# Kernel optimization log

Measured on AMD Instinct MI355X. Metric: run time of the kernel, lower is better.

## Reference

```python
import jax, jax.numpy as jnp
import numpy as np

EPS_OT = 0.05   # sinkhorn epsilon
ITERS = 3       # sinkhorn iterations
NH = 8          # attention heads


def _l2norm(x, axis):
    return x / jnp.maximum(jnp.linalg.norm(x, axis=axis, keepdims=True), 1e-12)


def _conv(x, w, pad):
    return jax.lax.conv_general_dilated(
        x, w, (1, 1), ((pad, pad), (pad, pad)),
        dimension_numbers=("NCHW", "OIHW", "NCHW"))


def _head(x, w1, b1, g, beta, w2, b2):
    # Conv3x3 -> BatchNorm (train-mode batch stats) -> ReLU -> Conv1x1
    h = _conv(x, w1, 1) + b1[None, :, None, None]
    mu = jnp.mean(h, (0, 2, 3), keepdims=True)
    var = jnp.var(h, (0, 2, 3), keepdims=True)
    h = jax.nn.relu((h - mu) / jnp.sqrt(var + 1e-5) * g[None, :, None, None]
                    + beta[None, :, None, None])
    return jnp.einsum("oc,bchw->bohw", w2, h) + b2[None, :, None, None]


def setup_inputs() -> dict:
    key = jax.random.key(0)
    ks = jax.random.split(key, 20)
    B, C, H, W, TD = 8, 256, 48, 48, 512
    s = 0.02
    f32 = jnp.float32
    d = {
        "img_feat": jax.random.normal(ks[0], (B, C, H, W), f32),
        "txt_feat": jax.random.normal(ks[1], (B, TD), f32),
        "density_map": jax.random.uniform(ks[2], (B, 1, H, W), f32),
        "tp_w": s * jax.random.normal(ks[3], (C, TD), f32), "tp_b": jnp.zeros((C,), f32),
        "wq": s * jax.random.normal(ks[4], (C, C), f32), "bq": jnp.zeros((C,), f32),
        "wk": s * jax.random.normal(ks[5], (C, C), f32), "bk": jnp.zeros((C,), f32),
        "wv": s * jax.random.normal(ks[6], (C, C), f32), "bv": jnp.zeros((C,), f32),
        "wo": s * jax.random.normal(ks[7], (C, C), f32), "bo": jnp.zeros((C,), f32),
        "ln_g": jnp.ones((C,), f32), "ln_b": jnp.zeros((C,), f32),
        "op_w": s * jax.random.normal(ks[8], (C, C), f32), "op_b": jnp.zeros((C,), f32),
        "h1_w": s * jax.random.normal(ks[9], (C // 2, C, 3, 3), f32), "h1_b": jnp.zeros((C // 2,), f32),
        "h_bn_g": jnp.ones((C // 2,), f32), "h_bn_b": jnp.zeros((C // 2,), f32),
        "h2_w": s * jax.random.normal(ks[10], (2, C // 2), f32), "h2_b": jnp.zeros((2,), f32),
        "v1_w": s * jax.random.normal(ks[11], (C // 2, C, 3, 3), f32), "v1_b": jnp.zeros((C // 2,), f32),
        "v_bn_g": jnp.ones((C // 2,), f32), "v_bn_b": jnp.zeros((C // 2,), f32),
        "v2_w": s * jax.random.normal(ks[12], (2, C // 2), f32), "v2_b": jnp.zeros((2,), f32),
        "temperature": 0.07 * jnp.ones((1,), f32),
        "spatial_weight": 0.1 * jnp.ones((1,), f32),
    }
    return d


def reference(img_feat, txt_feat, density_map, tp_w, tp_b, wq, bq, wk, bk,
              wv, bv, wo, bo, ln_g, ln_b, op_w, op_b, h1_w, h1_b, h_bn_g,
              h_bn_b, h2_w, h2_b, v1_w, v1_b, v_bn_g, v_bn_b, v2_w, v2_b,
              temperature, spatial_weight):
    B, C, H, W = img_feat.shape
    N = H * W
    hd = C // NH

    # ---- text projection (single text token) ----
    txt_emb = txt_feat @ tp_w.T + tp_b                      # [B,C]

    # ---- cross attention: query = pixels, key/value = 1 text token ----
    img_flat = img_feat.reshape(B, C, N).transpose(0, 2, 1)  # [B,N,C]
    q = (img_flat @ wq.T + bq).reshape(B, N, NH, hd)
    k = (txt_emb @ wk.T + bk).reshape(B, 1, NH, hd)
    v = (txt_emb @ wv.T + bv).reshape(B, 1, NH, hd)
    scores = jnp.einsum("bnhd,bkhd->bhnk", q, k) / jnp.sqrt(jnp.float32(hd))
    attn = jax.nn.softmax(scores, axis=-1)                  # ones (k len = 1)
    ctx = jnp.einsum("bhnk,bkhd->bnhd", attn, v).reshape(B, N, C)
    attn_out = ctx @ wo.T + bo

    # ---- residual + layernorm ----
    x = img_flat + attn_out
    mu = jnp.mean(x, -1, keepdims=True)
    var = jnp.var(x, -1, keepdims=True)
    source_feat = (x - mu) / jnp.sqrt(var + 1e-5) * ln_g + ln_b   # [B,N,C]
    mod_img_feat = source_feat.transpose(0, 2, 1).reshape(B, C, H, W)

    # ---- target distribution q from density map ----
    target = jax.nn.relu(density_map.reshape(B, N)) + 1e-6
    q_dist = target / jnp.sum(target, axis=1, keepdims=True)

    # ---- source distribution p from cosine similarity ----
    img_n = _l2norm(mod_img_feat, 1)                        # [B,C,H,W]
    txt_n = _l2norm(txt_emb, 1)                             # [B,C]
    cos = jnp.sum(img_n * txt_n[:, :, None, None], axis=1).reshape(B, N)
    temp = jnp.clip(temperature, 0.01, None)                # [1]
    logits = cos / temp
    mask = (cos > 0.0).astype(jnp.float32)
    shifted = logits - jnp.max(logits, axis=1, keepdims=True)
    p_un = jnp.exp(shifted) * mask + 1e-8
    p = p_un / jnp.sum(p_un, axis=1, keepdims=True)

    # ---- cost matrix: feature + spatial ----
    src_n = _l2norm(source_feat, 2)                         # [B,N,C]
    feature_cost = 1.0 - jnp.einsum("bnc,bmc->bnm", src_n, src_n)
    gy, gx = jnp.meshgrid(jnp.linspace(0.0, 1.0, H), jnp.linspace(0.0, 1.0, W),
                          indexing="ij")
    coords = jnp.stack([gy, gx], -1).reshape(N, 2)
    d2 = jnp.sum((coords[:, None, :] - coords[None, :, :]) ** 2, -1)
    spatial_cost = jnp.sqrt(jnp.maximum(d2, 0.0)) / 1.41421356  # [N,N]
    cost = feature_cost + spatial_weight * spatial_cost[None]   # [B,N,N]

    # ---- log-domain Sinkhorn ----
    log_p = jnp.log(p + 1e-12)
    log_q = jnp.log(q_dist + 1e-12)
    f = jnp.zeros_like(p)
    g = jnp.zeros_like(q_dist)
    for _ in range(ITERS):
        f = EPS_OT * (log_p - jax.scipy.special.logsumexp(
            (g[:, None, :] - cost) / EPS_OT, axis=2))
        g = EPS_OT * (log_q - jax.scipy.special.logsumexp(
            (f[:, :, None] - cost) / EPS_OT, axis=1))
    T = jnp.exp((f[:, :, None] + g[:, None, :] - cost) / EPS_OT)

    # ---- transport features: T^T @ source ----
    fused = jnp.einsum("bnm,bnc->bmc", T, source_feat)      # [B,N,C]
    fused_feat = fused.transpose(0, 2, 1).reshape(B, C, H, W)

    out_feat = img_feat + (jnp.einsum("oc,bchw->bohw", op_w, fused_feat)
                           + op_b[None, :, None, None])
    heatmap_logits = _head(out_feat, h1_w, h1_b, h_bn_g, h_bn_b, h2_w, h2_b)
    hv_logits = _head(out_feat, v1_w, v1_b, v_bn_g, v_bn_b, v2_w, v2_b)
    return out_feat, heatmap_logits, hv_logits
```

## Files before the change

kernel.cpp:

```cpp
#include <hip/hip_runtime.h>
#include <hip/hip_bf16.h>

#define NTOK 2304
#define CCH  256
#define BB   8
#define NSPL 2

typedef __attribute__((ext_vector_type(4))) float f32x4;
typedef __attribute__((ext_vector_type(8))) short s16x8;
typedef __attribute__((ext_vector_type(8))) _Float16 h16x8;
typedef unsigned short u16;
typedef unsigned char u8;

__device__ __forceinline__ u16 f2bf(float x){
  union{float f; unsigned u;} v; v.f = x;
  unsigned r = v.u + 0x7fffu + ((v.u>>16)&1u);
  return (u16)(r>>16);
}
__device__ __forceinline__ float bf2f(u16 h){
  union{float f; unsigned u;} v; v.u = ((unsigned)h)<<16; return v.f;
}

#if __has_builtin(__builtin_amdgcn_cvt_f32_fp8) && __has_builtin(__builtin_amdgcn_cvt_pk_fp8_f32)
#define HWFP8 1
#else
#define HWFP8 0
#endif

__device__ __forceinline__ u8 enc8(float z){
  union{float f; unsigned u;} a; a.f = fabsf(z) * 0x1p-120f;
  unsigned u = a.u + 0x7FFFFu + ((a.u>>20)&1u);
  unsigned b = (u>>20)&0x7Fu;
  if (b > 0x7Eu) b = 0x7Eu;
  return (u8)(b | (z<0.f ? 0x80u : 0u));
}
__device__ __forceinline__ float dec8(unsigned b){
  union{unsigned u; float f;} w;
  w.u = ((b&0x80u)<<24) | ((b&0x7Fu)<<20);
  return w.f * 0x1p120f;
}

#if HWFP8
__device__ __forceinline__ float DEC8(unsigned w, int e){
  switch(e & 3){
    case 0:  return __builtin_amdgcn_cvt_f32_fp8((int)w, 0);
    case 1:  return __builtin_amdgcn_cvt_f32_fp8((int)w, 1);
    case 2:  return __builtin_amdgcn_cvt_f32_fp8((int)w, 2);
    default: return __builtin_amdgcn_cvt_f32_fp8((int)w, 3);
  }
}
__device__ __forceinline__ unsigned pack4(float z0,float z1,float z2,float z3){
  int v = __builtin_amdgcn_cvt_pk_fp8_f32(z0, z1, 0, false);
  v = __builtin_amdgcn_cvt_pk_fp8_f32(z2, z3, v, true);
  return (unsigned)v;
}
#else
__device__ __forceinline__ float DEC8(unsigned w, int e){
  return dec8((w>>(8*(e&3)))&0xFFu);
}
__device__ __forceinline__ unsigned pack4(float z0,float z1,float z2,float z3){
  return (unsigned)enc8(z0) | ((unsigned)enc8(z1)<<8) |
         ((unsigned)enc8(z2)<<16) | ((unsigned)enc8(z3)<<24);
}
#endif

__device__ __forceinline__ int swz512(int row, int b){ return row*512 + (b ^ ((row&7)<<4)); }
__device__ __forceinline__ int swz128(int row, int b){ return row*128 + (b ^ ((row&7)<<4)); }
__device__ __forceinline__ int swz64 (int row, int b){ return row*64  + (b ^ ((row&3)<<4)); }

__device__ __forceinline__ void gl_lds16(const void* g, void* l){
  __builtin_amdgcn_global_load_lds(
      (const __attribute__((address_space(1))) unsigned int*)g,
      (__attribute__((address_space(3))) unsigned int*)l, 16, 0, 0);
}

struct CanonArgs {
  const void* src[31];
  int n[31];
  int off[31];
};

__global__ void k_detect(const u16* probe, int* flag){
  if (threadIdx.x==0){
    int cnt=0;
    for (int i=0;i<16;++i){
      unsigned e = (probe[2*i]>>7)&0xFFu;
      if (e>=100u && e<=140u) ++cnt;
    }
    *flag = (cnt>=14)?1:0;
  }
}

__global__ __launch_bounds__(256) void k_canon(CanonArgs a, float* dst, const int* flag, int nt){
  int t = blockIdx.y;
  if (t>=nt) return;
  int n = a.n[t];
  const void* s = a.src[t];
  float* d = dst + a.off[t];
  bool isbf = (*flag)!=0;
  int n4 = n >> 2;
  for (int i = blockIdx.x*256+threadIdx.x; i < n4; i += gridDim.x*256){
    if (isbf){
      ushort4 v = ((const ushort4*)s)[i];
      float4 o; o.x=bf2f(v.x); o.y=bf2f(v.y); o.z=bf2f(v.z); o.w=bf2f(v.w);
      ((float4*)d)[i] = o;
    } else {
      ((float4*)d)[i] = ((const float4*)s)[i];
    }
  }
  int base = n4<<2;
  int rem = n - base;
  int i = blockIdx.x*256+threadIdx.x;
  if (i < rem)
    d[base+i] = isbf ? bf2f(((const u16*)s)[base+i]) : ((const float*)s)[base+i];
}

__global__ __launch_bounds__(256) void k_zero(float* p, int n4){
  int i = blockIdx.x*256+threadIdx.x;
  if (i < n4) ((float4*)p)[i] = (float4){0.f,0.f,0.f,0.f};
}

__global__ __launch_bounds__(256) void k_txt(const float* txt, const float* tpw, const float* tpb,
    const float* wv, const float* bv, const float* wo, const float* bo, float* TXTN, float* AVEC){
  int b=blockIdx.x, t=threadIdx.x;
  __shared__ float sT[512];
  __shared__ float sE[256];
  __shared__ float sV[256];
  __shared__ float red[4];
  sT[t]      = txt[b*512+t];
  sT[t+256]  = txt[b*512+256+t];
  __syncthreads();
  float acc = tpb[t];
  const float* wr = tpw + (size_t)t*512;
  for (int k=0;k<512;++k) acc = fmaf(sT[k], wr[k], acc);
  sE[t] = acc;
  float ss = acc*acc;
  for (int d=1; d<64; d<<=1) ss += __shfl_xor(ss, d);
  if ((t&63)==0) red[t>>6] = ss;
  __syncthreads();
  float nrm = sqrtf(red[0]+red[1]+red[2]+red[3]);
  TXTN[b*256+t] = acc / fmaxf(nrm, 1e-12f);
  float av = bv[t];
  const float* wvr = wv + (size_t)t*256;
  for (int k=0;k<256;++k) av = fmaf(sE[k], wvr[k], av);
  sV[t] = av;
  __syncthreads();
  float ao = bo[t];
  const float* wor = wo + (size_t)t*256;
  for (int k=0;k<256;++k) ao = fmaf(sV[k], wor[k], ao);
  AVEC[b*256+t] = ao;
}

__global__ __launch_bounds__(256) void k_lnfuse(const float* img, const float* AVEC, const float* lng,
    const float* lnb, const float* TXTN, u16* SF, u16* SN, float* COS){
  int b=blockIdx.y, n0=blockIdx.x*32, t=threadIdx.x;
  __shared__ float xt[32][256];
  float av = AVEC[b*256+t];
  const float* ip = img + ((size_t)b*256 + t)*NTOK + n0;
  #pragma unroll
  for (int j4=0;j4<8;++j4){
    float4 v = *(const float4*)(ip + j4*4);
    xt[j4*4+0][t]=v.x+av; xt[j4*4+1][t]=v.y+av; xt[j4*4+2][t]=v.z+av; xt[j4*4+3][t]=v.w+av;
  }
  int wv_=t>>6, l=t&63;
  float lg[4], lb[4], tn[4];
  #pragma unroll
  for (int k=0;k<4;++k){ lg[k]=lng[l+64*k]; lb[k]=lnb[l+64*k]; tn[k]=TXTN[b*256+l+64*k]; }
  __syncthreads();
  for (int rr=0; rr<8; ++rr){
    int j = wv_*8+rr; int n = n0+j;
    float x[4]; float s=0.f, ss=0.f;
    #pragma unroll
    for (int k=0;k<4;++k){ float v=xt[j][l+64*k]; x[k]=v; s+=v; ss=fmaf(v,v,ss); }
    for (int d=1; d<64; d<<=1){ s += __shfl_xor(s,d); ss += __shfl_xor(ss,d); }
    float mu = s*(1.f/256.f);
    float var = ss*(1.f/256.f) - mu*mu;
    float rstd = rsqrtf(fmaxf(var,0.f)+1e-5f);
    float y[4]; float sy=0.f;
    #pragma unroll
    for (int k=0;k<4;++k){ y[k] = fmaf((x[k]-mu)*rstd, lg[k], lb[k]); sy = fmaf(y[k],y[k],sy); }
    for (int d=1; d<64; d<<=1) sy += __shfl_xor(sy,d);
    float rn = 1.f/fmaxf(sqrtf(sy),1e-12f);
    float cp = 0.f;
    size_t base = ((size_t)b*NTOK + n)*CCH;
    #pragma unroll
    for (int k=0;k<4;++k){
      float sv = y[k]*rn;
      SF[base + l+64*k] = f2bf(y[k]);
      SN[base + l+64*k] = f2bf(sv);
      cp = fmaf(sv, tn[k], cp);
    }
    for (int d=1; d<64; d<<=1) cp += __shfl_xor(cp,d);
    if (l==0) COS[b*NTOK+n] = cp;
  }
}

__global__ __launch_bounds__(256) void k_pqred(const float* COS, const float* den, const float* tmpp, float* PQS){
  int b=blockIdx.x, t=threadIdx.x;
  __shared__ float red[256];
  float temp = fmaxf(tmpp[0], 0.01f);
  float mx = -1e30f;
  for (int n=t; n<NTOK; n+=256) mx = fmaxf(mx, COS[b*NTOK+n]);
  red[t]=mx; __syncthreads();
  for (int o=128;o>0;o>>=1){ if (t<o) red[t]=fmaxf(red[t],red[t+o]); __syncthreads(); }
  float maxc = red[0]; __syncthreads();
  float sp=0.f, st=0.f;
  for (int n=t; n<NTOK; n+=256){
    float cv = COS[b*NTOK+n];
    sp += __expf((cv-maxc)/temp)*((cv>0.f)?1.f:0.f)+1e-8f;
    float dv = den[b*NTOK+n];
    st += fmaxf(dv,0.f)+1e-6f;
  }
  red[t]=sp; __syncthreads();
  for (int o=128;o>0;o>>=1){ if (t<o) red[t]+=red[t+o]; __syncthreads(); }
  sp = red[0]; __syncthreads();
  red[t]=st; __syncthreads();
  for (int o=128;o>0;o>>=1){ if (t<o) red[t]+=red[t+o]; __syncthreads(); }
  if (t==0){ PQS[b*4]=maxc; PQS[b*4+1]=sp; PQS[b*4+2]=red[0]; }
}

__global__ __launch_bounds__(256) void k_pqelem(const float* COS, const float* den, const float* tmpp,
    const float* PQS, float* LOGP, float* LOGQ, float* GV, float* CY, float* CX){
  int idx = blockIdx.x*256+threadIdx.x;
  float temp = fmaxf(tmpp[0], 0.01f);
  if (idx < BB*NTOK){
    int b = idx / NTOK;
    float maxc = PQS[b*4], sp = PQS[b*4+1], st = PQS[b*4+2];
    float cv = COS[idx];
    float pu = __expf((cv-maxc)/temp)*((cv>0.f)?1.f:0.f)+1e-8f;
    LOGP[idx] = logf(pu/sp + 1e-12f);
    float dv = den[idx];
    LOGQ[idx] = logf((fmaxf(dv,0.f)+1e-6f)/st + 1e-12f);
    GV[idx] = 0.f;
  }
  if (idx < NTOK){
    int h = idx/48, w = idx - h*48;
    CY[idx] = (float)h*(1.f/47.f);
    CX[idx] = (float)w*(1.f/47.f);
  }
}

__global__ __launch_bounds__(256) void k_packw(const float* h1w, const float* v1w, u16* W1P){
  int idx = blockIdx.x*256+threadIdx.x;
  int head = idx / 294912;
  int rem = idx - head*294912;
  int oc = rem / 2304;
  int k = rem - oc*2304;
  int tap = k >> 8;
  int c = k & 255;
  const float* src = head ? v1w : h1w;
  W1P[idx] = f2bf(src[(oc*256 + c)*9 + tap]);
}

__global__ __launch_bounds__(256) void k_trans(const u16* SF, u16* SFT){
  int n0 = blockIdx.x*64, c0 = blockIdx.y*64, b = blockIdx.z;
  __shared__ u16 tl[64][68];
  int t = threadIdx.x;
  int nl = t>>3, c8 = (t&7)*8;
  #pragma unroll
  for (int p=0;p<2;++p){
    int n = nl + p*32;
    s16x8 v = *(const s16x8*)(SF + ((size_t)(b*NTOK + n0+n)*CCH + c0 + c8));
    #pragma unroll
    for (int e=0;e<8;++e) tl[c8+e][n] = (u16)v[e];
  }
  __syncthreads();
  int cl = t>>3, n8 = (t&7)*8;
  #pragma unroll
  for (int p=0;p<2;++p){
    int c = cl + p*32;
    union{ s16x8 v; u16 us[8]; } pk;
    #pragma unroll
    for (int e=0;e<8;++e){ int s = n8+e; pk.us[e] = tl[c][((s&3)<<4) | (s>>2)]; }
    *(s16x8*)(SFT + ((size_t)(b*CCH + c0+c)*NTOK + n0 + n8)) = pk.v;
  }
}

__global__ __launch_bounds__(256, 4) void k_cost(const u16* SN, const float* CY, const float* CX,
    const float* swp, u8* Z, float* PZ, int b_base){
  int zb = blockIdx.z, b = b_base + zb;
  int i0 = blockIdx.x*64, by = blockIdx.y, j0b = by*256;
  const u16* SNb = SN + (size_t)b*NTOK*CCH;
  u8* Zb = Z + (size_t)zb*NTOK*NTOK;
  __shared__ __align__(16) char Bs[64*512];
  int tid=threadIdx.x, w=tid>>6, l=tid&63, g4=l>>4, lc=l&15;
  float spw = swp[0]*(20.0f/1.41421356f);
  const u16* Arow = SNb + (size_t)(i0 + w*16 + lc)*CCH + g4*8;
  s16x8 af[8];
  #pragma unroll
  for (int ks=0; ks<8; ++ks) af[ks] = *(const s16x8*)(Arow + ks*32);
  int mrow = w*16 + g4*4;
  float cyi[4], cxi[4];
  #pragma unroll
  for (int r=0;r<4;++r){ int i = i0+mrow+r; cyi[r]=CY[i]; cxi[r]=CX[i]; }
  float Srow[4] = {0.f,0.f,0.f,0.f};
  for (int js=0; js<4; ++js){
    int j0 = j0b + js*64;
    __syncthreads();
    #pragma unroll
    for (int u=0; u<8; ++u){
      int row = u*8 + w*2 + (l>>5);
      int src = ((l&31)*16) ^ ((row&7)<<4);
      gl_lds16((const char*)(SNb + (size_t)(j0+row)*CCH) + src, Bs + u*4096 + w*1024);
    }
    __syncthreads();
    f32x4 acc[4];
    #pragma unroll
    for (int cf=0;cf<4;++cf) acc[cf] = (f32x4){0.f,0.f,0.f,0.f};
    #pragma unroll
    for (int ks=0; ks<8; ++ks){
      int kb = ks*64 + g4*16;
      #pragma unroll
      for (int cf=0; cf<4; ++cf){
        s16x8 bb = *(const s16x8*)(Bs + swz512(cf*16+lc, kb));
        acc[cf] = __builtin_amdgcn_mfma_f32_16x16x32_bf16(af[ks], bb, acc[cf], 0,0,0);
      }
    }
    float zf[4][4];
    #pragma unroll
    for (int cf=0; cf<4; ++cf){
      int j = j0 + cf*16 + lc;
      float cyj = CY[j], cxj = CX[j];
      #pragma unroll
      for (int r=0;r<4;++r){
        float dy = cyi[r]-cyj, dx = cxi[r]-cxj;
        zf[cf][r] = (acc[cf][r]-1.0f)*20.0f - spw*sqrtf(fmaf(dy,dy,dx*dx));
      }
    }
    size_t zrow = (size_t)(i0+mrow)*NTOK + j0 + lc*4;
    #pragma unroll
    for (int r=0;r<4;++r){
      unsigned pw = pack4(zf[0][r], zf[1][r], zf[2][r], zf[3][r]);
      Srow[r] += __expf(DEC8(pw,0)) + __expf(DEC8(pw,1))
               + __expf(DEC8(pw,2)) + __expf(DEC8(pw,3));
      *(unsigned*)(Zb + zrow + (size_t)r*NTOK) = pw;
    }
  }
  #pragma unroll
  for (int r=0;r<4;++r){
    float s = Srow[r];
    s += __shfl_xor(s,1); s += __shfl_xor(s,2); s += __shfl_xor(s,4); s += __shfl_xor(s,8);
    if (lc==0) PZ[(size_t)(zb*NTOK + i0 + mrow + r)*9 + by] = s;
  }
}

__global__ __launch_bounds__(256) void k_sinkred(const float* PZ, const float* LOGP, float* FV,
    int b_base, int zcnt){
  int idx = blockIdx.x*256 + threadIdx.x;
  if (idx >= zcnt*NTOK) return;
  int zb = idx / NTOK, row = idx - zb*NTOK, b = b_base + zb;
  const float* p = PZ + (size_t)idx*9;
  float s = 0.f;
  #pragma unroll
  for (int k=0;k<9;++k) s += p[k];
  FV[b*NTOK+row] = 0.05f*(LOGP[b*NTOK+row] - logf(s));
}

__global__ __launch_bounds__(256) void k_sinkZ(const u8* Z, const float* addv,
    const float* basev, float* outv, int b_base){
  int zb = blockIdx.y, b = b_base + zb, i0 = blockIdx.x*32;
  __shared__ float fs[NTOK];
  __shared__ float wm[4];
  int t = threadIdx.x;
  for (int j=t; j<NTOK; j+=256){
    int p = j & 63, tt = ((p&3)<<4) | (p>>2);
    fs[j] = addv[b*NTOK + (j & ~63) + tt]*20.f;
  }
  __syncthreads();
  float m = -1e30f;
  for (int j=t; j<NTOK; j+=256) m = fmaxf(m, fs[j]);
  #pragma unroll
  for (int d=1; d<64; d<<=1) m = fmaxf(m, __shfl_xor(m, d));
  if ((t&63)==0) wm[t>>6] = m;
  __syncthreads();
  float C = fmaxf(fmaxf(wm[0],wm[1]), fmaxf(wm[2],wm[3]));
  int rl = t>>3, q = t&7;
  int row = i0 + rl;
  const u8* zr = Z + ((size_t)zb*NTOK + row)*NTOK;
  float S = 0.f;
  for (int c0 = q*32; c0 < NTOK; c0 += 256){
    uint4 zA = *(const uint4*)(zr + c0);
    uint4 zB = *(const uint4*)(zr + c0 + 16);
    unsigned wd[8] = {zA.x,zA.y,zA.z,zA.w, zB.x,zB.y,zB.z,zB.w};
    float s32 = 0.f;
    #pragma unroll
    for (int k=0;k<8;++k)
      #pragma unroll
      for (int e=0;e<4;++e)
        s32 += __expf(fs[c0 + k*4 + e] + DEC8(wd[k], e) - C);
    S += s32;
  }
  #pragma unroll
  for (int d=1; d<8; d<<=1) S += __shfl_xor(S, d);
  if (q==0)
    outv[b*NTOK+row] = 0.05f*(basev[b*NTOK+row] - (C + logf(S)));
}

__global__ __launch_bounds__(256, 3) void k_applyT(const u8* Z, const u16* SFT, const float* FVv,
    const float* GVv, float* FUF, int b_base){
  int zb = blockIdx.z, b = b_base + zb, m0 = blockIdx.x*64;
  int sp = blockIdx.y;
  int nbeg = sp*(NTOK/NSPL), nend = nbeg + (NTOK/NSPL);
  __shared__ __align__(16) char WtL[64*128];
  __shared__ __align__(16) char BL[256*128];
  __shared__ float gs[64];
  __shared__ float sfv[NTOK/NSPL];
  int tid=threadIdx.x, w=tid>>6, l=tid&63, g4=l>>4, lc=l&15;
  if (tid<64) gs[tid] = GVv[b*NTOK+m0+tid]*20.f;
  const float* Fv = FVv + b*NTOK;
  for (int j=tid; j<NTOK/NSPL; j+=256){
    int jj = nbeg + j;
    int p = jj & 63, tt = ((p&3)<<4) | (p>>2);
    sfv[j] = Fv[(jj & ~63) + tt]*20.f;
  }
  const u8* Zb = Z + ((size_t)zb*NTOK + m0)*NTOK;
  const u16* SFTb = SFT + (size_t)b*CCH*NTOK;
  f32x4 acc[4][4];
  #pragma unroll
  for (int mf=0;mf<4;++mf)
    #pragma unroll
    for (int cf=0;cf<4;++cf) acc[mf][cf] = (f32x4){0.f,0.f,0.f,0.f};
  int zm = tid>>2, zq = (tid&3)*16;
  int lrow = l>>3;
  int lsrc = ((l&7)*16) ^ (lrow<<4);
  uint4 zwc = *(const uint4*)(Zb + (size_t)zm*NTOK + nbeg + zq);
  for (int n0=nbeg; n0<nend; n0+=64){
    __syncthreads();
    int nn = (n0+64 < nend) ? n0+64 : nbeg;
    uint4 zwn = *(const uint4*)(Zb + (size_t)zm*NTOK + nn + zq);
    #pragma unroll
    for (int u=0; u<8; ++u){
      int row = w*64 + u*8 + lrow;
      gl_lds16((const char*)(SFTb + (size_t)row*NTOK) + n0*2 + lsrc,
               BL + (w*64 + u*8)*128);
    }
    {
      float g20 = gs[zm];
      unsigned wd[4] = {zwc.x, zwc.y, zwc.z, zwc.w};
      union{ s16x8 v; u16 us[8]; } w0, w1;
      int sbase = n0 - nbeg + zq;
      #pragma unroll
      for (int col=0; col<16; ++col){
        float val = __expf(sfv[sbase+col] + g20 + DEC8(wd[col>>2], col&3));
        if (col < 8) w0.us[col] = f2bf(val); else w1.us[col-8] = f2bf(val);
      }
      *(s16x8*)(WtL + swz128(zm, zq*2)) = w0.v;
      *(s16x8*)(WtL + swz128(zm, zq*2+16)) = w1.v;
    }
    __syncthreads();
    #pragma unroll
    for (int kk=0; kk<2; ++kk){
      s16x8 a[4];
      #pragma unroll
      for (int mf=0;mf<4;++mf) a[mf] = *(const s16x8*)(WtL + swz128(mf*16+lc, kk*64 + g4*16));
      #pragma unroll
      for (int cf=0; cf<4; ++cf){
        s16x8 bb = *(const s16x8*)(BL + swz128(w*64+cf*16+lc, kk*64 + g4*16));
        #pragma unroll
        for (int mf=0; mf<4; ++mf)
          acc[mf][cf] = __builtin_amdgcn_mfma_f32_16x16x32_bf16(a[mf], bb, acc[mf][cf], 0,0,0);
      }
    }
    zwc = zwn;
  }
  float* FUb = FUF + (size_t)b*NTOK*CCH;
  #pragma unroll
  for (int mf=0; mf<4; ++mf)
    #pragma unroll
    for (int cf=0; cf<4; ++cf)
      #pragma unroll
      for (int r=0;r<4;++r){
        int m = m0 + mf*16 + g4*4 + r;
        int c = w*64 + cf*16 + lc;
        atomicAdd(&FUb[(size_t)m*CCH + c], acc[mf][cf][r]);
      }
}

__global__ __launch_bounds__(256) void k_opgemm(const float* FUF, const float* opw, const float* opb,
    const float* img, float* dout, u16* OFN){
  int b=blockIdx.y, n0=blockIdx.x*64;
  __shared__ __align__(16) char Am[64*512];
  __shared__ __align__(16) char Bw[256*64];
  int tid=threadIdx.x, w=tid>>6, l=tid&63, g4=l>>4, lc=l&15;
  const float* FUb = FUF + (size_t)b*NTOK*CCH;
  for (int ch=tid; ch<64*32; ch+=256){
    int r=ch>>5, c8=(ch&31)*8;
    const float* fp = FUb + (size_t)(n0+r)*CCH + c8;
    float4 v0 = *(const float4*)fp;
    float4 v1 = *(const float4*)(fp+4);
    union { s16x8 v; u16 us[8]; } pk;
    pk.us[0]=f2bf(v0.x); pk.us[1]=f2bf(v0.y); pk.us[2]=f2bf(v0.z); pk.us[3]=f2bf(v0.w);
    pk.us[4]=f2bf(v1.x); pk.us[5]=f2bf(v1.y); pk.us[6]=f2bf(v1.z); pk.us[7]=f2bf(v1.w);
    *(s16x8*)(Am + swz512(r, c8*2)) = pk.v;
  }
  f32x4 acc[4][4];
  #pragma unroll
  for (int mf=0;mf<4;++mf)
    #pragma unroll
    for (int cf=0;cf<4;++cf) acc[mf][cf] = (f32x4){0.f,0.f,0.f,0.f};
  for (int ks=0; ks<8; ++ks){
    __syncthreads();
    {
      int o = tid;
      const float* wr = opw + (size_t)o*CCH + ks*32;
      #pragma unroll
      for (int u=0; u<4; ++u){
        float4 v0 = *(const float4*)(wr + u*8);
        float4 v1 = *(const float4*)(wr + u*8 + 4);
        union { s16x8 v; u16 us[8]; } pk;
        pk.us[0]=f2bf(v0.x); pk.us[1]=f2bf(v0.y); pk.us[2]=f2bf(v0.z); pk.us[3]=f2bf(v0.w);
        pk.us[4]=f2bf(v1.x); pk.us[5]=f2bf(v1.y); pk.us[6]=f2bf(v1.z); pk.us[7]=f2bf(v1.w);
        *(s16x8*)(Bw + swz64(o, u*16)) = pk.v;
      }
    }
    __syncthreads();
    #pragma unroll
    for (int mf=0; mf<4; ++mf){
      s16x8 a = *(const s16x8*)(Am + swz512(mf*16+lc, (ks*32+g4*8)*2));
      #pragma unroll
      for (int cf=0; cf<4; ++cf){
        int o = w*64+cf*16+lc;
        s16x8 bb = *(const s16x8*)(Bw + swz64(o, g4*16));
        acc[mf][cf] = __builtin_amdgcn_mfma_f32_16x16x32_bf16(a, bb, acc[mf][cf], 0,0,0);
      }
    }
  }
  #pragma unroll
  for (int mf=0; mf<4; ++mf){
    int nl = mf*16 + g4*4; int n = n0+nl;
    #pragma unroll
    for (int cf=0; cf<4; ++cf){
      int o = w*64+cf*16+lc;
      float ob = opb[o];
      const float* ip = img + ((size_t)b*CCH + o)*NTOK + n;
      float4 im = *(const float4*)ip;
      float o0 = acc[mf][cf][0]+ob+im.x;
      float o1 = acc[mf][cf][1]+ob+im.y;
      float o2 = acc[mf][cf][2]+ob+im.z;
      float o3 = acc[mf][cf][3]+ob+im.w;
      float4 st; st.x=o0; st.y=o1; st.z=o2; st.w=o3;
      *(float4*)(dout + ((size_t)b*CCH+o)*NTOK + n) = st;
      u16* ofp = OFN + ((size_t)b*NTOK + n)*CCH + o;
      ofp[0]=f2bf(o0); ofp[CCH]=f2bf(o1); ofp[2*CCH]=f2bf(o2); ofp[3*CCH]=f2bf(o3);
    }
  }
}

__global__ __launch_bounds__(256) void k_conv2(const u16* OFN, const u16* W1P,
    const float* h1b, const float* v1b, u16* H1, u16* H2){
  int b = blockIdx.y, n0 = blockIdx.x*64;
  __shared__ __align__(16) char As[64*128];
  __shared__ __align__(16) char Ws[256*128];
  int tid=threadIdx.x, w=tid>>6, l=tid&63, g4=l>>4, lc=l&15;
  int ar = tid>>2, aseg = (tid&3)*16;
  int arow = n0 + ar;
  int hr = arow/48, wc = arow - hr*48;
  const u16* Ob = OFN + (size_t)b*NTOK*CCH;
  const u16* Wg = W1P + (size_t)tid*2304;
  f32x4 acc[4][4];
  #pragma unroll
  for (int mf=0;mf<4;++mf)
    #pragma unroll
    for (int of=0;of<4;++of) acc[mf][of] = (f32x4){0.f,0.f,0.f,0.f};
  for (int kc=0; kc<36; ++kc){
    int tap = kc>>2, cq = (kc&3)*64;
    int kh = tap/3;
    int dh = kh-1, dw = (tap-kh*3)-1;
    bool val = ((unsigned)(hr+dh) < 48u) && ((unsigned)(wc+dw) < 48u);
    s16x8 a0 = {0,0,0,0,0,0,0,0}, a1 = {0,0,0,0,0,0,0,0};
    if (val){
      const u16* ap = Ob + (size_t)(arow + dh*48 + dw)*CCH + cq + aseg;
      a0 = *(const s16x8*)ap;
      a1 = *(const s16x8*)(ap+8);
    }
    const u16* wp = Wg + tap*256 + cq;
    s16x8 wv[8];
    #pragma unroll
    for (int u=0;u<8;++u) wv[u] = *(const s16x8*)(wp + u*8);
    __syncthreads();
    *(s16x8*)(As + swz128(ar, aseg*2))    = a0;
    *(s16x8*)(As + swz128(ar, aseg*2+16)) = a1;
    #pragma unroll
    for (int u=0;u<8;++u) *(s16x8*)(Ws + swz128(tid, u*16)) = wv[u];
    __syncthreads();
    #pragma unroll
    for (int ks=0; ks<2; ++ks){
      s16x8 af[4];
      #pragma unroll
      for (int mf=0;mf<4;++mf) af[mf] = *(const s16x8*)(As + swz128(mf*16+lc, ks*64 + g4*16));
      #pragma unroll
      for (int of=0; of<4; ++of){
        s16x8 bf = *(const s16x8*)(Ws + swz128(w*64+of*16+lc, ks*64 + g4*16));
        #pragma unroll
        for (int mf=0; mf<4; ++mf)
          acc[mf][of] = __builtin_amdgcn_mfma_f32_16x16x32_bf16(af[mf], bf, acc[mf][of], 0,0,0);
      }
    }
  }
  #pragma unroll
  for (int of=0; of<4; ++of){
    int o = w*64 + of*16 + lc;
    int head = o>>7, oc = o&127;
    float bias = (head? v1b : h1b)[oc];
    u16* Hh = head? H2 : H1;
    #pragma unroll
    for (int mf=0; mf<4; ++mf){
      #pragma unroll
      for (int r=0;r<4;++r){
        int n = n0 + mf*16 + g4*4 + r;
        Hh[((size_t)b*NTOK+n)*128 + oc] = f2bf(acc[mf][of][r] + bias);
      }
    }
  }
}

__global__ __launch_bounds__(128) void k_stats(const u16* H1, const u16* H2, float* PART){
  int head=blockIdx.y, blk=blockIdx.x, t=threadIdx.x;
  const u16* Hh = head? H2:H1;
  float s=0.f, ss=0.f;
  size_t r0 = (size_t)blk*288;
  for (int r=0;r<288;++r){
    float v = bf2f(Hh[(r0+r)*128 + t]);
    s += v; ss = fmaf(v,v,ss);
  }
  PART[((head*64+blk)*128+t)*2]   = s;
  PART[((head*64+blk)*128+t)*2+1] = ss;
}

__global__ __launch_bounds__(128) void k_statr(const float* PART, const float* hbg, const float* hbb,
    const float* vbg, const float* vbb, float* BNS){
  int head=blockIdx.x, t=threadIdx.x;
  float s=0.f, ss=0.f;
  for (int blk=0;blk<64;++blk){
    s  += PART[((head*64+blk)*128+t)*2];
    ss += PART[((head*64+blk)*128+t)*2+1];
  }
  float mean = s*(1.f/18432.f);
  float var = ss*(1.f/18432.f) - mean*mean;
  var = fmaxf(var, 0.f);
  const float* g  = head? vbg:hbg;
  const float* be = head? vbb:hbb;
  float sc = g[t]/sqrtf(var+1e-5f);
  BNS[(head*128+t)*2]   = sc;
  BNS[(head*128+t)*2+1] = be[t] - mean*sc;
}

__global__ __launch_bounds__(128) void k_fin(const u16* H1, const u16* H2, const float* BNS,
    const float* h2w, const float* h2b, const float* v2w, const float* v2b, float* dout){
  int head = blockIdx.z, b = blockIdx.y, n0 = blockIdx.x*128, t=threadIdx.x;
  const u16* Hh = head? H2:H1;
  const float* w2 = head? v2w:h2w;
  const float* b2 = head? v2b:h2b;
  __shared__ u16 tile[128][130];
  __shared__ float sc[128], bi[128], wa[128], wb[128];
  sc[t]=BNS[(head*128+t)*2]; bi[t]=BNS[(head*128+t)*2+1];
  wa[t]=w2[t]; wb[t]=w2[128+t];
  for (int r=0;r<128;++r) tile[r][t] = Hh[((size_t)b*NTOK+n0+r)*128 + t];
  __syncthreads();
  float a0=b2[0], a1=b2[1];
  for (int ch=0; ch<128; ++ch){
    float v = fmaf(bf2f(tile[t][ch]), sc[ch], bi[ch]);
    v = fmaxf(v, 0.f);
    a0 = fmaf(wa[ch], v, a0);
    a1 = fmaf(wb[ch], v, a1);
  }
  size_t base = (size_t)8*256*2304 + (size_t)head*36864 + (size_t)b*2*2304 + n0 + t;
  dout[base]        = a0;
  dout[base+2304]   = a1;
}

extern "C" void kernel_launch(void* const* d_in, const int* in_sizes, int n_in,
                              void* d_out, int out_size, void* d_ws, size_t ws_size,
                              hipStream_t stream){
  (void)out_size;
  long off[31]; long tot=0;
  int ni = n_in < 31 ? n_in : 31;
  for (int i=0;i<ni;++i){ off[i]=tot; tot += ((long)in_sizes[i]+63)&~63L; }
  char* ws = (char*)d_ws;
  size_t pos = 0;
  auto alloc = [&](size_t bytes)->char*{
    char* p = ws+pos; pos = (pos + bytes + 255) & ~(size_t)255; return p; };
  int*   FLAG = (int*)alloc(256);
  float* TXTN = (float*)alloc(8*256*4);
  float* AVEC = (float*)alloc(8*256*4);
  float* COS  = (float*)alloc(8*2304*4);
  float* LOGP = (float*)alloc(8*2304*4);
  float* LOGQ = (float*)alloc(8*2304*4);
  float* FV   = (float*)alloc(8*2304*4);
  float* GV   = (float*)alloc(8*2304*4);
  float* CY   = (float*)alloc(2304*4);
  float* CX   = (float*)alloc(2304*4);
  float* PQS  = (float*)alloc(8*4*4);
  float* PART = (float*)alloc(2*64*128*2*4);
  float* BNS  = (float*)alloc(2*128*2*4);
  float* PZ   = (float*)alloc((size_t)8*2304*9*4);
  u16* W1P = (u16*)alloc((size_t)2*128*9*256*2);
  u16* SF  = (u16*)alloc((size_t)8*2304*256*2);
  u16* SN  = (u16*)alloc((size_t)8*2304*256*2);
  u16* SFT = (u16*)alloc((size_t)8*2304*256*2);
  float* FUF = (float*)alloc((size_t)8*2304*256*4);
  u16* OFN = (u16*)alloc((size_t)8*2304*256*2);
  u16* H1  = (u16*)alloc((size_t)8*2304*128*2);
  u16* H2  = (u16*)alloc((size_t)8*2304*128*2);
  float* canon = (float*)alloc((size_t)tot*4);
  size_t zslice = (size_t)NTOK*NTOK;
  int zsl = (pos + 8*zslice + 256 <= ws_size) ? 8 : 1;
  u8* Z = (u8*)alloc((size_t)zsl*zslice);

  k_detect<<<1,64,0,stream>>>((const u16*)d_in[1], FLAG);
  CanonArgs ca;
  for (int i=0;i<ni;++i){ ca.src[i]=d_in[i]; ca.n[i]=in_sizes[i]; ca.off[i]=(int)off[i]; }
  k_canon<<<dim3(512,(unsigned)ni),256,0,stream>>>(ca, canon, FLAG, ni);
  k_zero<<<4608,256,0,stream>>>(FUF, 8*2304*256/4);

  const float* c_img = canon+off[0];
  const float* c_txt = canon+off[1];
  const float* c_den = canon+off[2];
  const float* c_tpw = canon+off[3];
  const float* c_tpb = canon+off[4];
  const float* c_wv  = canon+off[9];
  const float* c_bv  = canon+off[10];
  const float* c_wo  = canon+off[11];
  const float* c_bo  = canon+off[12];
  const float* c_lng = canon+off[13];
  const float* c_lnb = canon+off[14];
  const float* c_opw = canon+off[15];
  const float* c_opb = canon+off[16];
  const float* c_h1w = canon+off[17];
  const float* c_h1b = canon+off[18];
  const float* c_hbg = canon+off[19];
  const float* c_hbb = canon+off[20];
  const float* c_h2w = canon+off[21];
  const float* c_h2b = canon+off[22];
  const float* c_v1w = canon+off[23];
  const float* c_v1b = canon+off[24];
  const float* c_vbg = canon+off[25];
  const float* c_vbb = canon+off[26];
  const float* c_v2w = canon+off[27];
  const float* c_v2b = canon+off[28];
  const float* c_tmp = canon+off[29];
  const float* c_sw  = canon+off[30];

  k_txt<<<8,256,0,stream>>>(c_txt, c_tpw, c_tpb, c_wv, c_bv, c_wo, c_bo, TXTN, AVEC);
  k_lnfuse<<<dim3(72,8),256,0,stream>>>(c_img, AVEC, c_lng, c_lnb, TXTN, SF, SN, COS);
  k_pqred<<<8,256,0,stream>>>(COS, c_den, c_tmp, PQS);
  k_pqelem<<<80,256,0,stream>>>(COS, c_den, c_tmp, PQS, LOGP, LOGQ, GV, CY, CX);
  k_packw<<<2304,256,0,stream>>>(c_h1w, c_v1w, W1P);
  k_trans<<<dim3(36,4,8),256,0,stream>>>(SF, SFT);

  if (zsl == 8){
    k_cost<<<dim3(36,9,8),256,0,stream>>>(SN, CY, CX, c_sw, Z, PZ, 0);
    k_sinkred<<<72,256,0,stream>>>(PZ, LOGP, FV, 0, 8);
    for (int it=0; it<3; ++it){
      if (it>0) k_sinkZ<<<dim3(72,8),256,0,stream>>>(Z, GV, LOGP, FV, 0);
      k_sinkZ<<<dim3(72,8),256,0,stream>>>(Z, FV, LOGQ, GV, 0);
    }
    k_applyT<<<dim3(36,NSPL,8),256,0,stream>>>(Z, SFT, FV, GV, FUF, 0);
  } else {
    for (int bi=0; bi<8; ++bi){
      k_cost<<<dim3(36,9,1),256,0,stream>>>(SN, CY, CX, c_sw, Z, PZ, bi);
      k_sinkred<<<9,256,0,stream>>>(PZ, LOGP, FV, bi, 1);
      for (int it=0; it<3; ++it){
        if (it>0) k_sinkZ<<<dim3(72,1),256,0,stream>>>(Z, GV, LOGP, FV, bi);
        k_sinkZ<<<dim3(72,1),256,0,stream>>>(Z, FV, LOGQ, GV, bi);
      }
      k_applyT<<<dim3(36,NSPL,1),256,0,stream>>>(Z, SFT, FV, GV, FUF, bi);
    }
  }

  k_opgemm<<<dim3(36,8),256,0,stream>>>(FUF, c_opw, c_opb, c_img, (float*)d_out, OFN);
  k_conv2<<<dim3(36,8),256,0,stream>>>(OFN, W1P, c_h1b, c_v1b, H1, H2);
  k_stats<<<dim3(64,2),128,0,stream>>>(H1, H2, PART);
  k_statr<<<2,128,0,stream>>>(PART, c_hbg, c_hbb, c_vbg, c_vbb, BNS);
  k_fin<<<dim3(18,8,2),128,0,stream>>>(H1, H2, BNS, c_h2w, c_h2b, c_v2w, c_v2b, (float*)d_out);
}
```

Baseline: 412.0 us.

## Split conv3x3 reduction across two blocks with atomics and register prefetch

The 3x3 conv GEMM now splits its 36 K-chunks across two blocks (grid z=2), which doubles the block count from 288 to 576 to fill more CUs. Partial sums are accumulated with float atomicAdd into a zeroed fp32 scratch buffer that reuses FUF, and a new k_hfin kernel adds the bias and converts to bf16 H1/H2. The main loop also prefetches the next chunk's global loads into registers while the current chunk is staged in shared memory. In exchange it adds a zeroing kernel, a finalize kernel, heavy scattered atomic traffic (one scalar atomic per output element per split), and nondeterministic summation order.

```diff
diff --git a/kernel.cpp b/kernel.cpp
--- a/kernel.cpp
+++ b/kernel.cpp
@@ -546,9 +546,9 @@
   }
 }
 
-__global__ __launch_bounds__(256) void k_conv2(const u16* OFN, const u16* W1P,
-    const float* h1b, const float* v1b, u16* H1, u16* H2){
-  int b = blockIdx.y, n0 = blockIdx.x*64;
+__global__ __launch_bounds__(256, 2) void k_conv2(const u16* OFN, const u16* W1P, float* HF){
+  int b = blockIdx.y, n0 = blockIdx.x*64, spk = blockIdx.z;
+  int kbeg = spk*18, kend = kbeg+18;
   __shared__ __align__(16) char As[64*128];
   __shared__ __align__(16) char Ws[256*128];
   int tid=threadIdx.x, w=tid>>6, l=tid&63, g4=l>>4, lc=l&15;
@@ -562,26 +562,32 @@
   for (int mf=0;mf<4;++mf)
     #pragma unroll
     for (int of=0;of<4;++of) acc[mf][of] = (f32x4){0.f,0.f,0.f,0.f};
-  for (int kc=0; kc<36; ++kc){
+  auto LOADK = [&](int kc, s16x8& ra0, s16x8& ra1, s16x8* rwv){
     int tap = kc>>2, cq = (kc&3)*64;
     int kh = tap/3;
     int dh = kh-1, dw = (tap-kh*3)-1;
     bool val = ((unsigned)(hr+dh) < 48u) && ((unsigned)(wc+dw) < 48u);
-    s16x8 a0 = {0,0,0,0,0,0,0,0}, a1 = {0,0,0,0,0,0,0,0};
+    ra0 = (s16x8){0,0,0,0,0,0,0,0}; ra1 = ra0;
     if (val){
       const u16* ap = Ob + (size_t)(arow + dh*48 + dw)*CCH + cq + aseg;
-      a0 = *(const s16x8*)ap;
-      a1 = *(const s16x8*)(ap+8);
+      ra0 = *(const s16x8*)ap;
+      ra1 = *(const s16x8*)(ap+8);
     }
     const u16* wp = Wg + tap*256 + cq;
-    s16x8 wv[8];
-    #pragma unroll
-    for (int u=0;u<8;++u) wv[u] = *(const s16x8*)(wp + u*8);
+    #pragma unroll
+    for (int u=0;u<8;++u) rwv[u] = *(const s16x8*)(wp + u*8);
+  };
+  s16x8 a0, a1, wv[8];
+  LOADK(kbeg, a0, a1, wv);
+  for (int kc=kbeg; kc<kend; ++kc){
     __syncthreads();
     *(s16x8*)(As + swz128(ar, aseg*2))    = a0;
     *(s16x8*)(As + swz128(ar, aseg*2+16)) = a1;
     #pragma unroll
     for (int u=0;u<8;++u) *(s16x8*)(Ws + swz128(tid, u*16)) = wv[u];
+    s16x8 na0, na1, nwv[8];
+    int nk = (kc+1 < kend) ? kc+1 : kbeg;
+    LOADK(nk, na0, na1, nwv);
     __syncthreads();
     #pragma unroll
     for (int ks=0; ks<2; ++ks){
@@ -596,22 +602,37 @@
           acc[mf][of] = __builtin_amdgcn_mfma_f32_16x16x32_bf16(af[mf], bf, acc[mf][of], 0,0,0);
       }
     }
+    a0 = na0; a1 = na1;
+    #pragma unroll
+    for (int u=0;u<8;++u) wv[u] = nwv[u];
   }
   #pragma unroll
   for (int of=0; of<4; ++of){
     int o = w*64 + of*16 + lc;
-    int head = o>>7, oc = o&127;
-    float bias = (head? v1b : h1b)[oc];
-    u16* Hh = head? H2 : H1;
     #pragma unroll
     for (int mf=0; mf<4; ++mf){
       #pragma unroll
       for (int r=0;r<4;++r){
         int n = n0 + mf*16 + g4*4 + r;
-        Hh[((size_t)b*NTOK+n)*128 + oc] = f2bf(acc[mf][of][r] + bias);
-      }
-    }
-  }
+        atomicAdd(&HF[((size_t)(b*NTOK+n))*CCH + o], acc[mf][of][r]);
+      }
+    }
+  }
+}
+
+__global__ __launch_bounds__(256) void k_hfin(const float* HF, const float* h1b, const float* v1b,
+    u16* H1, u16* H2){
+  int idx = (blockIdx.x*256+threadIdx.x)*4;
+  int o = idx & 255; int bn = idx >> 8;
+  int head = o>>7, oc = o&127;
+  const float* bp = head? v1b : h1b;
+  float4 v = *(const float4*)(HF + idx);
+  ushort4 st;
+  st.x = f2bf(v.x + bp[oc]);
+  st.y = f2bf(v.y + bp[oc+1]);
+  st.z = f2bf(v.z + bp[oc+2]);
+  st.w = f2bf(v.w + bp[oc+3]);
+  *(ushort4*)((head? H2:H1) + (size_t)bn*128 + oc) = st;
 }
 
 __global__ __launch_bounds__(128) void k_stats(const u16* H1, const u16* H2, float* PART){
@@ -769,7 +790,9 @@
   }
 
   k_opgemm<<<dim3(36,8),256,0,stream>>>(FUF, c_opw, c_opb, c_img, (float*)d_out, OFN);
-  k_conv2<<<dim3(36,8),256,0,stream>>>(OFN, W1P, c_h1b, c_v1b, H1, H2);
+  k_zero<<<4608,256,0,stream>>>(FUF, 8*2304*256/4);
+  k_conv2<<<dim3(36,8,2),256,0,stream>>>(OFN, W1P, FUF);
+  k_hfin<<<4608,256,0,stream>>>(FUF, c_h1b, c_v1b, H1, H2);
   k_stats<<<dim3(64,2),128,0,stream>>>(H1, H2, PART);
   k_statr<<<2,128,0,stream>>>(PART, c_hbg, c_hbb, c_vbg, c_vbb, BNS);
   k_fin<<<dim3(18,8,2),128,0,stream>>>(H1, H2, BNS, c_h2w, c_h2b, c_v2w, c_v2b, (float*)d_out);
```

Result: slower. 426.2 us (+3.4%).

## Double-buffer conv weights via direct global-to-LDS loads with chunk-major packing

Applied to the files above, without the earlier changes.

The 3x3 conv weights are repacked into chunk-major order so each K-chunk is one contiguous 32KB block, pre-swizzled for the LDS layout. k_conv2 now stages the next chunk's weights straight into a second LDS buffer with global-to-LDS loads, and prefetches the next activation tile into registers while the current chunk's MFMAs run. The intent is to hide global load latency behind compute and to drop the register round trip for weights. It doubles weight LDS use to 64KB and depends on hand-placed barriers and waitcnt being correct.

```diff
diff --git a/kernel.cpp b/kernel.cpp
--- a/kernel.cpp
+++ b/kernel.cpp
@@ -240,16 +240,17 @@
   }
 }
 
-__global__ __launch_bounds__(256) void k_packw(const float* h1w, const float* v1w, u16* W1P){
+__global__ __launch_bounds__(256) void k_packw(const float* h1w, const float* v1w, u16* W2P){
   int idx = blockIdx.x*256+threadIdx.x;
-  int head = idx / 294912;
-  int rem = idx - head*294912;
-  int oc = rem / 2304;
-  int k = rem - oc*2304;
-  int tap = k >> 8;
-  int c = k & 255;
+  int kc = idx >> 14;
+  int rem = idx & 16383;
+  int o = rem >> 6;
+  int cl = rem & 63;
+  int tap = kc >> 2;
+  int c = ((kc&3)<<6) + cl;
+  int head = o >> 7, oc = o & 127;
   const float* src = head ? v1w : h1w;
-  W1P[idx] = f2bf(src[(oc*256 + c)*9 + tap]);
+  W2P[idx] = f2bf(src[(oc*256 + c)*9 + tap]);
 }
 
 __global__ __launch_bounds__(256) void k_trans(const u16* SF, u16* SFT){
@@ -546,43 +547,58 @@
   }
 }
 
-__global__ __launch_bounds__(256) void k_conv2(const u16* OFN, const u16* W1P,
+__global__ __launch_bounds__(256, 2) void k_conv2(const u16* OFN, const u16* W2P,
     const float* h1b, const float* v1b, u16* H1, u16* H2){
   int b = blockIdx.y, n0 = blockIdx.x*64;
   __shared__ __align__(16) char As[64*128];
-  __shared__ __align__(16) char Ws[256*128];
+  __shared__ __align__(16) char Ws[2][256*128];
   int tid=threadIdx.x, w=tid>>6, l=tid&63, g4=l>>4, lc=l&15;
   int ar = tid>>2, aseg = (tid&3)*16;
   int arow = n0 + ar;
   int hr = arow/48, wc = arow - hr*48;
   const u16* Ob = OFN + (size_t)b*NTOK*CCH;
-  const u16* Wg = W1P + (size_t)tid*2304;
+  int wrow = tid>>3;
+  int wsrc = ((tid&7)*16) ^ ((wrow&7)<<4);
+  const char* Wbase = (const char*)W2P;
   f32x4 acc[4][4];
   #pragma unroll
   for (int mf=0;mf<4;++mf)
     #pragma unroll
     for (int of=0;of<4;++of) acc[mf][of] = (f32x4){0.f,0.f,0.f,0.f};
-  for (int kc=0; kc<36; ++kc){
+  auto STAGEW = [&](int kc, int buf){
+    const char* src = Wbase + (size_t)kc*32768;
+    #pragma unroll
+    for (int u=0; u<8; ++u)
+      gl_lds16(src + (size_t)(u*32 + wrow)*128 + wsrc, Ws[buf] + u*4096 + w*1024);
+  };
+  auto LOADA = [&](int kc, s16x8& ra0, s16x8& ra1){
     int tap = kc>>2, cq = (kc&3)*64;
     int kh = tap/3;
     int dh = kh-1, dw = (tap-kh*3)-1;
     bool val = ((unsigned)(hr+dh) < 48u) && ((unsigned)(wc+dw) < 48u);
-    s16x8 a0 = {0,0,0,0,0,0,0,0}, a1 = {0,0,0,0,0,0,0,0};
+    ra0 = (s16x8){0,0,0,0,0,0,0,0}; ra1 = ra0;
     if (val){
       const u16* ap = Ob + (size_t)(arow + dh*48 + dw)*CCH + cq + aseg;
-      a0 = *(const s16x8*)ap;
-      a1 = *(const s16x8*)(ap+8);
-    }
-    const u16* wp = Wg + tap*256 + cq;
-    s16x8 wv[8];
-    #pragma unroll
-    for (int u=0;u<8;++u) wv[u] = *(const s16x8*)(wp + u*8);
-    __syncthreads();
+      ra0 = *(const s16x8*)ap;
+      ra1 = *(const s16x8*)(ap+8);
+    }
+  };
+  s16x8 a0, a1, na0, na1;
+  STAGEW(0, 0);
+  LOADA(0, a0, a1);
+  for (int kc=0; kc<36; ++kc){
+    int cur = kc & 1;
+    __builtin_amdgcn_s_barrier();
+    __builtin_amdgcn_sched_barrier(0);
+    if (kc+1 < 36){
+      STAGEW(kc+1, cur^1);
+      LOADA(kc+1, na0, na1);
+    }
     *(s16x8*)(As + swz128(ar, aseg*2))    = a0;
     *(s16x8*)(As + swz128(ar, aseg*2+16)) = a1;
-    #pragma unroll
-    for (int u=0;u<8;++u) *(s16x8*)(Ws + swz128(tid, u*16)) = wv[u];
-    __syncthreads();
+    asm volatile("s_waitcnt lgkmcnt(0)" ::: "memory");
+    __builtin_amdgcn_s_barrier();
+    __builtin_amdgcn_sched_barrier(0);
     #pragma unroll
     for (int ks=0; ks<2; ++ks){
       s16x8 af[4];
@@ -590,12 +606,13 @@
       for (int mf=0;mf<4;++mf) af[mf] = *(const s16x8*)(As + swz128(mf*16+lc, ks*64 + g4*16));
       #pragma unroll
       for (int of=0; of<4; ++of){
-        s16x8 bf = *(const s16x8*)(Ws + swz128(w*64+of*16+lc, ks*64 + g4*16));
+        s16x8 bf = *(const s16x8*)(Ws[cur] + swz128(w*64+of*16+lc, ks*64 + g4*16));
         #pragma unroll
         for (int mf=0; mf<4; ++mf)
           acc[mf][of] = __builtin_amdgcn_mfma_f32_16x16x32_bf16(af[mf], bf, acc[mf][of], 0,0,0);
       }
     }
+    a0 = na0; a1 = na1;
   }
   #pragma unroll
   for (int of=0; of<4; ++of){
@@ -694,7 +711,7 @@
   float* PART = (float*)alloc(2*64*128*2*4);
   float* BNS  = (float*)alloc(2*128*2*4);
   float* PZ   = (float*)alloc((size_t)8*2304*9*4);
-  u16* W1P = (u16*)alloc((size_t)2*128*9*256*2);
+  u16* W2P = (u16*)alloc((size_t)36*256*64*2);
   u16* SF  = (u16*)alloc((size_t)8*2304*256*2);
   u16* SN  = (u16*)alloc((size_t)8*2304*256*2);
   u16* SFT = (u16*)alloc((size_t)8*2304*256*2);
@@ -745,7 +762,7 @@
   k_lnfuse<<<dim3(72,8),256,0,stream>>>(c_img, AVEC, c_lng, c_lnb, TXTN, SF, SN, COS);
   k_pqred<<<8,256,0,stream>>>(COS, c_den, c_tmp, PQS);
   k_pqelem<<<80,256,0,stream>>>(COS, c_den, c_tmp, PQS, LOGP, LOGQ, GV, CY, CX);
-  k_packw<<<2304,256,0,stream>>>(c_h1w, c_v1w, W1P);
+  k_packw<<<2304,256,0,stream>>>(c_h1w, c_v1w, W2P);
   k_trans<<<dim3(36,4,8),256,0,stream>>>(SF, SFT);
 
   if (zsl == 8){
@@ -769,7 +786,7 @@
   }
 
   k_opgemm<<<dim3(36,8),256,0,stream>>>(FUF, c_opw, c_opb, c_img, (float*)d_out, OFN);
-  k_conv2<<<dim3(36,8),256,0,stream>>>(OFN, W1P, c_h1b, c_v1b, H1, H2);
+  k_conv2<<<dim3(36,8),256,0,stream>>>(OFN, W2P, c_h1b, c_v1b, H1, H2);
   k_stats<<<dim3(64,2),128,0,stream>>>(H1, H2, PART);
   k_statr<<<2,128,0,stream>>>(PART, c_hbg, c_hbb, c_vbg, c_vbb, BNS);
   k_fin<<<dim3(18,8,2),128,0,stream>>>(H1, H2, BNS, c_h2w, c_h2b, c_v2w, c_v2b, (float*)d_out);
```

Result: faster. 385.9 us (-6.4%).
